# Kernel optimization log

Hardware: AMD Instinct MI355X
Metric: run time of the kernel (lower is better)

## Reference

```python
import jax, jax.numpy as jnp
import numpy as np

NEG_INF = -1.0e9
LN_EPS = 1e-5
LEAK = 0.2


def setup_inputs() -> dict:
    key = jax.random.key(0)
    ks = jax.random.split(key, 8)
    B, C, T, N, H = 8, 64, 24, 512, 2
    hd = C // H
    x = jax.random.normal(ks[0], (B, C, T, N), dtype=jnp.float32)
    gso = jax.random.randint(ks[1], (N, N), 0, 2, dtype=jnp.int32)
    # torch nn.Linear weights are (out, in); xavier-ish scale
    s = (2.0 / (C + C)) ** 0.5
    Wq = jax.random.normal(ks[2], (C, C), dtype=jnp.float32) * s
    Wk = jax.random.normal(ks[3], (C, C), dtype=jnp.float32) * s
    Wv = jax.random.normal(ks[4], (C, C), dtype=jnp.float32) * s
    sa = (2.0 / (H + hd)) ** 0.5
    a_src = jax.random.normal(ks[5], (H, hd), dtype=jnp.float32) * sa
    a_dst = jax.random.normal(ks[6], (H, hd), dtype=jnp.float32) * sa
    ln_gamma = jnp.ones((C,), dtype=jnp.float32)
    ln_beta = jnp.zeros((C,), dtype=jnp.float32)
    return {"x": x, "gso": gso, "Wq": Wq, "Wk": Wk, "Wv": Wv,
            "a_src": a_src, "a_dst": a_dst, "ln_gamma": ln_gamma, "ln_beta": ln_beta}


def _spatial_gat(x, gso, Wq, Wk, Wv, a_src, a_dst, ln_gamma, ln_beta):
    B, C, T, N = x.shape
    H, hd = a_src.shape
    # (B, C, T, N) -> (B*T, N, C)
    xr = jnp.transpose(x, (0, 2, 3, 1)).reshape(B * T, N, C)
    # torch Linear: y = x @ W.T
    Q = jnp.einsum('bnc,dc->bnd', xr, Wq).reshape(B * T, N, H, hd)
    K = jnp.einsum('bnc,dc->bnd', xr, Wk).reshape(B * T, N, H, hd)
    V = jnp.einsum('bnc,dc->bnd', xr, Wv).reshape(B * T, N, H, hd)
    # additive GAT scores, all heads at once
    s_src = jnp.einsum('bnhd,hd->bnh', Q, a_src)  # (BT, N, H)
    s_dst = jnp.einsum('bnhd,hd->bnh', K, a_dst)  # (BT, N, H)
    scores = jax.nn.leaky_relu(s_src[:, :, None, :] + s_dst[:, None, :, :], LEAK)  # (BT, Ni, Nj, H)
    mask = jnp.where(gso == 0, jnp.float32(NEG_INF), jnp.float32(0.0))  # (N, N)
    scores = scores + mask[None, :, :, None]
    attn = jax.nn.softmax(scores, axis=2)  # softmax over destination j
    out = jnp.einsum('bijh,bjhd->bihd', attn, V)  # (BT, N, H, hd)
    out = out.reshape(B * T, N, C)
    # LayerNorm over channel dim
    mu = jnp.mean(out, axis=-1, keepdims=True)
    var = jnp.var(out, axis=-1, keepdims=True)
    out = (out - mu) * jax.lax.rsqrt(var + LN_EPS) * ln_gamma + ln_beta
    # back to (B, C, T, N)
    return jnp.transpose(out.reshape(B, T, N, C), (0, 3, 1, 2))


def reference(x, gso, Wq, Wk, Wv, a_src, a_dst, ln_gamma, ln_beta):
    return _spatial_gat(x, gso, Wq, Wk, Wv, a_src, a_dst, ln_gamma, ln_beta)
```

## Files before the change

kernel.cpp:

```cpp
#include <hip/hip_runtime.h>

#define CDIM 64
#define TDIM 24
#define NDIM 512
#define NBT  192

typedef float    float4v __attribute__((ext_vector_type(4)));
typedef _Float16 half8v  __attribute__((ext_vector_type(8)));
typedef _Float16 half2v  __attribute__((ext_vector_type(2)));


__global__ void k0_prep(const int* __restrict__ gso,
                        const float* __restrict__ Wq, const float* __restrict__ Wk,
                        const float* __restrict__ a_src, const float* __restrict__ a_dst,
                        unsigned* __restrict__ maskb, float* __restrict__ wfold) {
  int t = threadIdx.x;
  if (blockIdx.x < 256) {
    int tg = blockIdx.x * 256 + t;
    int4 g = ((const int4*)gso)[tg];
    unsigned w = (g.x ? 0x000000FFu : 0u) | (g.y ? 0x0000FF00u : 0u) |
                 (g.z ? 0x00FF0000u : 0u) | (g.w ? 0xFF000000u : 0u);
    maskb[tg] = w;
  } else {
    int r = t >> 6, c = t & 63;
    const float* av = (r & 2) ? a_dst : a_src;
    const float* W  = (r & 2) ? Wk : Wq;
    int off = (r & 1) * 32;
    float s = 0.f;
#pragma unroll
    for (int d = 0; d < 32; ++d)
      s += av[off + d] * W[(off + d) * 64 + c];
    wfold[t] = s;
  }
}

struct SmemK1 {
  union {
    _Float16 xt[128][72];
    _Float16 vtb[64][136];
  } big;
  _Float16 wv[64][72];
  _Float16 wext[16][72];
};

__launch_bounds__(256, 4)
__global__ void k1_v(const float* __restrict__ x, const float* __restrict__ Wv,
                     const float* __restrict__ wfold,
                     _Float16* __restrict__ VT_g,
                     float* __restrict__ s_src_g, float* __restrict__ s_dst_g) {
  __shared__ SmemK1 sm;
  const int t  = threadIdx.x;
  const int qn = blockIdx.x;
  const int bt = blockIdx.y;
  const int b  = bt / TDIM, tt = bt % TDIM;
  const int n0 = qn * 128;

  for (int it = 0; it < 16; ++it) {
    int idx = it * 256 + t;
    sm.wv[idx >> 6][idx & 63] = (_Float16)Wv[idx];
  }
  for (int z = t; z < 12 * 72; z += 256) ((_Float16*)sm.wext[4])[z] = (_Float16)0.f;
  {
    int r = t >> 6, c = t & 63;
    sm.wext[r][c] = (_Float16)wfold[t];
  }
  for (int it = 0; it < 16; ++it) {
    int idx = it * 256 + t;
    int cp = idx >> 7, n = idx & 127;
    int c0 = cp * 2;
    const float* base = x + ((size_t)(b * CDIM + c0) * TDIM + tt) * NDIM + n0 + n;
    half2v p; p[0] = (_Float16)base[0]; p[1] = (_Float16)base[(size_t)TDIM * NDIM];
    *(half2v*)&sm.big.xt[n][c0] = p;
  }
  __syncthreads();

  const int lane = t & 63, w = t >> 6;
  const int m = lane & 15, quad = lane >> 4;
  const int mbase = w * 32;

  float4v acc[2][5];
#pragma unroll
  for (int mt = 0; mt < 2; ++mt)
#pragma unroll
    for (int nt = 0; nt < 5; ++nt)
#pragma unroll
      for (int r = 0; r < 4; ++r) acc[mt][nt][r] = 0.f;

#pragma unroll
  for (int ks = 0; ks < 2; ++ks) {
    half8v af[2], bf[5];
#pragma unroll
    for (int mt = 0; mt < 2; ++mt)
      af[mt] = *(const half8v*)&sm.big.xt[mbase + mt * 16 + m][ks * 32 + quad * 8];
#pragma unroll
    for (int nt = 0; nt < 4; ++nt)
      bf[nt] = *(const half8v*)&sm.wv[nt * 16 + m][ks * 32 + quad * 8];
    bf[4] = *(const half8v*)&sm.wext[m][ks * 32 + quad * 8];
#pragma unroll
    for (int mt = 0; mt < 2; ++mt)
#pragma unroll
      for (int nt = 0; nt < 5; ++nt)
        acc[mt][nt] = __builtin_amdgcn_mfma_f32_16x16x32_f16(af[mt], bf[nt], acc[mt][nt], 0, 0, 0);
  }

  if (m < 4) {
    float* basep = (m < 2 ? s_src_g : s_dst_g) + (size_t)(bt * 2 + (m & 1)) * NDIM;
#pragma unroll
    for (int mt = 0; mt < 2; ++mt)
#pragma unroll
      for (int r = 0; r < 4; ++r)
        basep[n0 + mbase + mt * 16 + quad * 4 + r] = acc[mt][4][r];
  }
  __syncthreads();

#pragma unroll
  for (int mt = 0; mt < 2; ++mt)
#pragma unroll
    for (int nt = 0; nt < 4; ++nt)
#pragma unroll
      for (int r = 0; r < 4; r += 2) {
        int nl = mbase + mt * 16 + quad * 4 + r;
        int c  = nt * 16 + m;
        half2v p = __builtin_bit_cast(half2v,
            __builtin_amdgcn_cvt_pkrtz(acc[mt][nt][r], acc[mt][nt][r + 1]));
        *(half2v*)&sm.big.vtb[c][nl] = p;
      }
  __syncthreads();

  const unsigned* vdw = (const unsigned*)sm.big.vtb;
  unsigned* outdw = (unsigned*)VT_g;
  for (int it = 0; it < 16; ++it) {
    int idx = it * 256 + t;
    int c = idx >> 6, jd = idx & 63;
    outdw[(size_t)(bt * 64 + c) * 256 + qn * 64 + jd] = vdw[c * 68 + jd];
  }
}

struct SmemK2 {
  union {
    struct { _Float16 vt[64][128]; unsigned char mb[64][144]; } s;
    struct { float otile[64][66]; float rsum[4][64]; float rsq[4][64];
             float mu[64]; float rs[64]; } e;
  } u;
  float sdst[2][512];
};

__launch_bounds__(256, 4)
__global__ void k2_attn(const _Float16* __restrict__ VT_g,
                        const float* __restrict__ s_src_g, const float* __restrict__ s_dst_g,
                        const unsigned char* __restrict__ maskb,
                        const float* __restrict__ gamma, const float* __restrict__ beta,
                        float* __restrict__ out) {
  __shared__ SmemK2 sm;
  const int t     = threadIdx.x;
  const int itile = blockIdx.x;
  const int bt    = blockIdx.y;
  const int i0    = itile * 64;
  const int b     = bt / TDIM, tt = bt % TDIM;
  const int lane  = t & 63, w = t >> 6;
  const int h = w >> 1, ihalf = w & 1;
  const int m = lane & 15, quad = lane >> 4;

  for (int it = 0; it < 4; ++it) {
    int idx = it * 256 + t;
    ((float*)sm.sdst)[idx] = s_dst_g[(size_t)bt * 2 * NDIM + idx];
  }
  float s1r[2], s2r[2];
#pragma unroll
  for (int mt = 0; mt < 2; ++mt) {
    float sv = s_src_g[(size_t)(bt * 2 + h) * NDIM + i0 + ihalf * 32 + mt * 16 + m];
    s1r[mt] = sv - 4.f;
    s2r[mt] = 0.2f * sv - 4.f;
  }

  float4v acc[2][2], accs[2];
#pragma unroll
  for (int mt = 0; mt < 2; ++mt) {
#pragma unroll
    for (int r = 0; r < 4; ++r) { acc[mt][0][r] = 0.f; acc[mt][1][r] = 0.f; accs[mt][r] = 0.f; }
  }
  const half8v bones = {(_Float16)1.f, (_Float16)1.f, (_Float16)1.f, (_Float16)1.f,
                        (_Float16)1.f, (_Float16)1.f, (_Float16)1.f, (_Float16)1.f};

  for (int js = 0; js < 4; ++js) {
    __syncthreads();
    {
      const uint4* vsrc = (const uint4*)VT_g;
#pragma unroll
      for (int it = 0; it < 4; ++it) {
        int idx = it * 256 + t;
        int c = idx >> 4, ch = idx & 15;
        uint4 val = vsrc[(size_t)(bt * 64 + c) * 64 + js * 16 + ch];
        *(uint4*)&sm.u.s.vt[c][(ch * 8) ^ ((c & 7) * 8)] = val;
      }
#pragma unroll
      for (int it = 0; it < 2; ++it) {
        int idx = it * 256 + t;
        int c = idx >> 3, ch = idx & 7;
        uint4 mv = *(const uint4*)(maskb + (size_t)(i0 + c) * NDIM + js * 128 + ch * 16);
        *(uint4*)&sm.u.s.mb[c][ch * 16] = mv;
      }
    }
    __syncthreads();

#pragma unroll
    for (int ksl = 0; ksl < 4; ++ksl) {
      int jq = ksl * 32 + quad * 8;
      float4v dj0 = *(const float4v*)&sm.sdst[h][js * 128 + jq];
      float4v dj1 = *(const float4v*)&sm.sdst[h][js * 128 + jq + 4];
      int vbase = (h * 32 + m) * 128 + (jq ^ ((m & 7) * 8));
      half8v b0 = *(const half8v*)&sm.u.s.vt[0][vbase];
      half8v b1 = *(const half8v*)&sm.u.s.vt[0][vbase + 16 * 128];
#pragma unroll
      for (int mt = 0; mt < 2; ++mt) {
        const unsigned* mwp = (const unsigned*)&sm.u.s.mb[ihalf * 32 + mt * 16 + m][jq];
        unsigned mw0 = mwp[0], mw1 = mwp[1];
        float e[8];
#pragma unroll
        for (int jj = 0; jj < 8; ++jj) {
          float d = (jj < 4) ? dj0[jj] : dj1[jj - 4];
          float f1 = s1r[mt] + d;
          float f2 = __builtin_fmaf(d, 0.2f, s2r[mt]);
          e[jj] = __expf(fmaxf(f1, f2));
        }
        unsigned p0 = __builtin_bit_cast(unsigned, __builtin_amdgcn_cvt_pkrtz(e[0], e[1]))
                      & __builtin_amdgcn_perm(0u, mw0, 0x01010000u);
        unsigned p1 = __builtin_bit_cast(unsigned, __builtin_amdgcn_cvt_pkrtz(e[2], e[3]))
                      & __builtin_amdgcn_perm(0u, mw0, 0x03030202u);
        unsigned p2 = __builtin_bit_cast(unsigned, __builtin_amdgcn_cvt_pkrtz(e[4], e[5]))
                      & __builtin_amdgcn_perm(0u, mw1, 0x01010000u);
        unsigned p3 = __builtin_bit_cast(unsigned, __builtin_amdgcn_cvt_pkrtz(e[6], e[7]))
                      & __builtin_amdgcn_perm(0u, mw1, 0x03030202u);
        uint4 au; au.x = p0; au.y = p1; au.z = p2; au.w = p3;
        half8v af = __builtin_bit_cast(half8v, au);
        acc[mt][0] = __builtin_amdgcn_mfma_f32_16x16x32_f16(af, b0,    acc[mt][0], 0, 0, 0);
        acc[mt][1] = __builtin_amdgcn_mfma_f32_16x16x32_f16(af, b1,    acc[mt][1], 0, 0, 0);
        accs[mt]   = __builtin_amdgcn_mfma_f32_16x16x32_f16(af, bones, accs[mt],   0, 0, 0);
      }
    }
  }

  __syncthreads();
#pragma unroll
  for (int mt = 0; mt < 2; ++mt)
#pragma unroll
    for (int r = 0; r < 4; ++r) {
      float sc = __builtin_amdgcn_rcpf(accs[mt][r]);
      int i_loc = ihalf * 32 + mt * 16 + quad * 4 + r;
#pragma unroll
      for (int nt = 0; nt < 2; ++nt)
        sm.u.e.otile[i_loc][h * 32 + nt * 16 + m] = acc[mt][nt][r] * sc;
    }
  __syncthreads();

  {
    int i = t & 63, cg = t >> 6;
    float s1 = 0.f, s2 = 0.f;
#pragma unroll
    for (int cc = 0; cc < 16; ++cc) {
      float v = sm.u.e.otile[i][cg * 16 + cc];
      s1 += v; s2 += v * v;
    }
    sm.u.e.rsum[cg][i] = s1;
    sm.u.e.rsq[cg][i]  = s2;
  }
  __syncthreads();
  if (t < 64) {
    int i = t;
    float s1 = 0.f, s2 = 0.f;
#pragma unroll
    for (int cg = 0; cg < 4; ++cg) { s1 += sm.u.e.rsum[cg][i]; s2 += sm.u.e.rsq[cg][i]; }
    float mu  = s1 * (1.f / 64.f);
    float var = s2 * (1.f / 64.f) - mu * mu;
    sm.u.e.mu[i] = mu;
    sm.u.e.rs[i] = rsqrtf(var + 1e-5f);
  }
  __syncthreads();
  {
    int i = t & 63, cg = t >> 6;
    float mu = sm.u.e.mu[i], rs = sm.u.e.rs[i];
    int n = i0 + i;
#pragma unroll
    for (int cc = 0; cc < 16; ++cc) {
      int c = cg * 16 + cc;
      float v = (sm.u.e.otile[i][c] - mu) * rs * gamma[c] + beta[c];
      out[((size_t)(b * CDIM + c) * TDIM + tt) * NDIM + n] = v;
    }
  }
}

extern "C" void kernel_launch(void* const* d_in, const int* in_sizes, int n_in,
                              void* d_out, int out_size, void* d_ws, size_t ws_size,
                              hipStream_t stream) {
  const float* x     = (const float*)d_in[0];
  const int*   gso   = (const int*)d_in[1];
  const float* Wq    = (const float*)d_in[2];
  const float* Wk    = (const float*)d_in[3];
  const float* Wv    = (const float*)d_in[4];
  const float* a_src = (const float*)d_in[5];
  const float* a_dst = (const float*)d_in[6];
  const float* gamma = (const float*)d_in[7];
  const float* beta  = (const float*)d_in[8];
  float* out = (float*)d_out;

  char* ws = (char*)d_ws;
  _Float16* VT_g  = (_Float16*)ws;
  float*    s_src = (float*)(ws + 12582912);
  float*    s_dst = (float*)(ws + 13369344);
  unsigned char* maskb = (unsigned char*)(ws + 14155776);
  float*    wfold = (float*)(ws + 14417920);

  k0_prep<<<257, 256, 0, stream>>>(gso, Wq, Wk, a_src, a_dst, (unsigned*)maskb, wfold);
  k1_v<<<dim3(4, NBT), 256, 0, stream>>>(x, Wv, wfold, VT_g, s_src, s_dst);
  k2_attn<<<dim3(8, NBT), 256, 0, stream>>>(VT_g, s_src, s_dst, maskb, gamma, beta, out);
}
```

Measured before the change: 130.4 us.

## Factor exponentials into per-row and per-column terms, prepack fp16 weights

Because exp is monotonic, exp(leaky_relu(s+d)) equals max(exp(s)*exp(d), exp(0.2s)*exp(0.2d)). The attention kernel now precomputes base-2 exponentials of the source and destination scores once, and the inner loop uses two multiplies and a max instead of a per-element exp. The folded attention vectors are pre-scaled by log2(e) so exp2 can be used. Separately, the prep kernel packs Wv and the folded vectors into one fp16 buffer that k1 copies with vector loads, and the LDS row pitch shrinks from 72 to 68. Precomputing the exponentials risks overflow or underflow in fp32 and fp16, since the -6 offset replaces the earlier -4 shift.

```diff
diff --git a/kernel.cpp b/kernel.cpp
--- a/kernel.cpp
+++ b/kernel.cpp
@@ -7,13 +7,29 @@
 
 typedef float    float4v __attribute__((ext_vector_type(4)));
 typedef _Float16 half8v  __attribute__((ext_vector_type(8)));
+typedef _Float16 half4v  __attribute__((ext_vector_type(4)));
 typedef _Float16 half2v  __attribute__((ext_vector_type(2)));
 
+
+__device__ __forceinline__ float exp2_fast(float x) {
+#if __has_builtin(__builtin_amdgcn_exp2f)
+  return __builtin_amdgcn_exp2f(x);
+#else
+  return __expf(x * 0.69314718f);
+#endif
+}
+
+__device__ __forceinline__ half8v ld8(const _Float16* p) {
+  half4v a = *(const half4v*)p;
+  half4v b = *(const half4v*)(p + 4);
+  return __builtin_shufflevector(a, b, 0, 1, 2, 3, 4, 5, 6, 7);
+}
 
 __global__ void k0_prep(const int* __restrict__ gso,
                         const float* __restrict__ Wq, const float* __restrict__ Wk,
+                        const float* __restrict__ Wv,
                         const float* __restrict__ a_src, const float* __restrict__ a_dst,
-                        unsigned* __restrict__ maskb, float* __restrict__ wfold) {
+                        unsigned* __restrict__ maskb, _Float16* __restrict__ wvext_g) {
   int t = threadIdx.x;
   if (blockIdx.x < 256) {
     int tg = blockIdx.x * 256 + t;
@@ -22,30 +38,39 @@
                  (g.z ? 0x00FF0000u : 0u) | (g.w ? 0xFF000000u : 0u);
     maskb[tg] = w;
   } else {
-    int r = t >> 6, c = t & 63;
-    const float* av = (r & 2) ? a_dst : a_src;
-    const float* W  = (r & 2) ? Wk : Wq;
-    int off = (r & 1) * 32;
-    float s = 0.f;
-#pragma unroll
-    for (int d = 0; d < 32; ++d)
-      s += av[off + d] * W[(off + d) * 64 + c];
-    wfold[t] = s;
+    for (int idx = t; idx < 80 * 68; idx += 256) {
+      int row = idx / 68, col = idx - row * 68;
+      float v = 0.f;
+      if (col < 64) {
+        if (row < 64) {
+          v = Wv[row * 64 + col];
+        } else if (row < 68) {
+          int r = row - 64;
+          const float* av = (r & 2) ? a_dst : a_src;
+          const float* W  = (r & 2) ? Wk : Wq;
+          int off = (r & 1) * 32;
+          float s = 0.f;
+#pragma unroll
+          for (int d = 0; d < 32; ++d)
+            s += av[off + d] * W[(off + d) * 64 + col];
+          v = s * 1.44269504f;
+        }
+      }
+      wvext_g[idx] = (_Float16)v;
+    }
   }
 }
 
 struct SmemK1 {
   union {
-    _Float16 xt[128][72];
+    _Float16 xt[128][68];
     _Float16 vtb[64][136];
   } big;
-  _Float16 wv[64][72];
-  _Float16 wext[16][72];
+  _Float16 wvext[80][68];
 };
 
 __launch_bounds__(256, 4)
-__global__ void k1_v(const float* __restrict__ x, const float* __restrict__ Wv,
-                     const float* __restrict__ wfold,
+__global__ void k1_v(const float* __restrict__ x, const _Float16* __restrict__ wvext_g,
                      _Float16* __restrict__ VT_g,
                      float* __restrict__ s_src_g, float* __restrict__ s_dst_g) {
   __shared__ SmemK1 sm;
@@ -55,14 +80,14 @@
   const int b  = bt / TDIM, tt = bt % TDIM;
   const int n0 = qn * 128;
 
-  for (int it = 0; it < 16; ++it) {
-    int idx = it * 256 + t;
-    sm.wv[idx >> 6][idx & 63] = (_Float16)Wv[idx];
-  }
-  for (int z = t; z < 12 * 72; z += 256) ((_Float16*)sm.wext[4])[z] = (_Float16)0.f;
   {
-    int r = t >> 6, c = t & 63;
-    sm.wext[r][c] = (_Float16)wfold[t];
+    const uint4* wsrc = (const uint4*)wvext_g;
+    uint4* wdst = (uint4*)sm.wvext;
+#pragma unroll
+    for (int it = 0; it < 3; ++it) {
+      int idx = it * 256 + t;
+      if (idx < 680) wdst[idx] = wsrc[idx];
+    }
   }
   for (int it = 0; it < 16; ++it) {
     int idx = it * 256 + t;
@@ -91,11 +116,11 @@
     half8v af[2], bf[5];
 #pragma unroll
     for (int mt = 0; mt < 2; ++mt)
-      af[mt] = *(const half8v*)&sm.big.xt[mbase + mt * 16 + m][ks * 32 + quad * 8];
+      af[mt] = ld8(&sm.big.xt[mbase + mt * 16 + m][ks * 32 + quad * 8]);
 #pragma unroll
     for (int nt = 0; nt < 4; ++nt)
-      bf[nt] = *(const half8v*)&sm.wv[nt * 16 + m][ks * 32 + quad * 8];
-    bf[4] = *(const half8v*)&sm.wext[m][ks * 32 + quad * 8];
+      bf[nt] = ld8(&sm.wvext[nt * 16 + m][ks * 32 + quad * 8]);
+    bf[4] = ld8(&sm.wvext[64 + m][ks * 32 + quad * 8]);
 #pragma unroll
     for (int mt = 0; mt < 2; ++mt)
 #pragma unroll
@@ -142,7 +167,8 @@
     struct { float otile[64][66]; float rsum[4][64]; float rsq[4][64];
              float mu[64]; float rs[64]; } e;
   } u;
-  float sdst[2][512];
+  float sF[2][512];
+  float sFp[2][512];
 };
 
 __launch_bounds__(256, 4)
@@ -163,14 +189,16 @@
 
   for (int it = 0; it < 4; ++it) {
     int idx = it * 256 + t;
-    ((float*)sm.sdst)[idx] = s_dst_g[(size_t)bt * 2 * NDIM + idx];
-  }
-  float s1r[2], s2r[2];
+    float d = s_dst_g[(size_t)bt * 2 * NDIM + idx];
+    ((float*)sm.sF)[idx]  = exp2_fast(d);
+    ((float*)sm.sFp)[idx] = exp2_fast(0.2f * d);
+  }
+  float E[2], Ep[2];
 #pragma unroll
   for (int mt = 0; mt < 2; ++mt) {
     float sv = s_src_g[(size_t)(bt * 2 + h) * NDIM + i0 + ihalf * 32 + mt * 16 + m];
-    s1r[mt] = sv - 4.f;
-    s2r[mt] = 0.2f * sv - 4.f;
+    E[mt]  = exp2_fast(sv - 6.f);
+    Ep[mt] = exp2_fast(0.2f * sv - 6.f);
   }
 
   float4v acc[2][2], accs[2];
@@ -206,8 +234,10 @@
 #pragma unroll
     for (int ksl = 0; ksl < 4; ++ksl) {
       int jq = ksl * 32 + quad * 8;
-      float4v dj0 = *(const float4v*)&sm.sdst[h][js * 128 + jq];
-      float4v dj1 = *(const float4v*)&sm.sdst[h][js * 128 + jq + 4];
+      float4v F0 = *(const float4v*)&sm.sF[h][js * 128 + jq];
+      float4v F1 = *(const float4v*)&sm.sF[h][js * 128 + jq + 4];
+      float4v P0 = *(const float4v*)&sm.sFp[h][js * 128 + jq];
+      float4v P1 = *(const float4v*)&sm.sFp[h][js * 128 + jq + 4];
       int vbase = (h * 32 + m) * 128 + (jq ^ ((m & 7) * 8));
       half8v b0 = *(const half8v*)&sm.u.s.vt[0][vbase];
       half8v b1 = *(const half8v*)&sm.u.s.vt[0][vbase + 16 * 128];
@@ -218,10 +248,9 @@
         float e[8];
 #pragma unroll
         for (int jj = 0; jj < 8; ++jj) {
-          float d = (jj < 4) ? dj0[jj] : dj1[jj - 4];
-          float f1 = s1r[mt] + d;
-          float f2 = __builtin_fmaf(d, 0.2f, s2r[mt]);
-          e[jj] = __expf(fmaxf(f1, f2));
+          float Fv = (jj < 4) ? F0[jj] : F1[jj - 4];
+          float Pv = (jj < 4) ? P0[jj] : P1[jj - 4];
+          e[jj] = fmaxf(E[mt] * Fv, Ep[mt] * Pv);
         }
         unsigned p0 = __builtin_bit_cast(unsigned, __builtin_amdgcn_cvt_pkrtz(e[0], e[1]))
                       & __builtin_amdgcn_perm(0u, mw0, 0x01010000u);
@@ -308,9 +337,9 @@
   float*    s_src = (float*)(ws + 12582912);
   float*    s_dst = (float*)(ws + 13369344);
   unsigned char* maskb = (unsigned char*)(ws + 14155776);
-  float*    wfold = (float*)(ws + 14417920);
-
-  k0_prep<<<257, 256, 0, stream>>>(gso, Wq, Wk, a_src, a_dst, (unsigned*)maskb, wfold);
-  k1_v<<<dim3(4, NBT), 256, 0, stream>>>(x, Wv, wfold, VT_g, s_src, s_dst);
+  _Float16* wvext = (_Float16*)(ws + 14417920);
+
+  k0_prep<<<257, 256, 0, stream>>>(gso, Wq, Wk, Wv, a_src, a_dst, (unsigned*)maskb, wvext);
+  k1_v<<<dim3(4, NBT), 256, 0, stream>>>(x, wvext, VT_g, s_src, s_dst);
   k2_attn<<<dim3(8, NBT), 256, 0, stream>>>(VT_g, s_src, s_dst, maskb, gamma, beta, out);
 }
```

New measurement: 137.1 us. +5.1%, slower.
